# Performance work log

Measured on AMD Instinct MI355X. Metric: run time of the kernel, lower is better.

The kernel has to match this reference:

```python
import jax, jax.numpy as jnp
import numpy as np

B, IC, N = 32, 1, 64
KN, KS, PAD = 128, 65, 16
R, LAT = 8, 32
LEAK = 0.01
THETA_PRIOR = float(np.pi)
HW = N + 2 * PAD - KS + 1  # 32
OFFSETS = np.array([0, np.pi/4, np.pi/2, 3*np.pi/4, np.pi, -3*np.pi/4, -np.pi/2, -np.pi/4], dtype=np.float32)


def rotate_filters(w, n_rot):
    """Bilinear rotation of [O,I,k,k] filters for n_rot angles, matching
    F.affine_grid/F.grid_sample with align_corners=False, zero padding.
    Returns [O*n_rot, I, k, k] (rotation-major within each O block)."""
    O, I, k, _ = w.shape
    thetas = (2.0 * jnp.pi / n_rot) * jnp.arange(n_rot, dtype=jnp.float32)
    coords = (2.0 * jnp.arange(k, dtype=jnp.float32) + 1.0) / k - 1.0  # normalized, align_corners=False
    yy, xx = jnp.meshgrid(coords, coords, indexing='ij')  # [k,k]
    cos = jnp.cos(thetas)[:, None, None]
    sin = jnp.sin(thetas)[:, None, None]
    xs = cos * xx + sin * yy   # [R,k,k] sample x (normalized)
    ys = -sin * xx + cos * yy  # [R,k,k] sample y
    px = ((xs + 1.0) * k - 1.0) * 0.5  # pixel coords
    py = ((ys + 1.0) * k - 1.0) * 0.5
    x0 = jnp.floor(px); y0 = jnp.floor(py)
    wx = px - x0; wy = py - y0

    def gather(yi, xi):
        valid = (yi >= 0) & (yi < k) & (xi >= 0) & (xi < k)
        yc = jnp.clip(yi, 0, k - 1).astype(jnp.int32)
        xc = jnp.clip(xi, 0, k - 1).astype(jnp.int32)
        v = w[:, :, yc, xc]  # [O,I,R,k,k]
        return v * valid.astype(w.dtype)

    out = (gather(y0, x0) * (1 - wy) * (1 - wx)
           + gather(y0, x0 + 1) * (1 - wy) * wx
           + gather(y0 + 1, x0) * wy * (1 - wx)
           + gather(y0 + 1, x0 + 1) * wy * wx)  # [O,I,R,k,k]
    return jnp.transpose(out, (0, 2, 1, 3, 4)).reshape(O * n_rot, I, k, k)


def conv1x1(h, w, b):
    # h: [B,C,R,H,W], w: [O,C], b: [O] -- Conv3d with 1x1x1 kernel
    return jnp.einsum('bcrhw,oc->borhw', h, w) + b[None, :, None, None, None]


def _forward(x, w1, b1, w2, b2, wa, ba, wr, br, wz, bz, gumbel):
    tw = rotate_filters(w1[:, :, 0], R)  # [KN*R, IC, KS, KS]
    y = jax.lax.conv_general_dilated(
        x, tw, window_strides=(1, 1), padding=[(PAD, PAD), (PAD, PAD)],
        dimension_numbers=('NCHW', 'OIHW', 'NCHW'))
    Bn = y.shape[0]
    y = y.reshape(Bn, KN, R, HW, HW) + b1[None, :, None, None, None]
    xa = jax.nn.leaky_relu(y, LEAK)
    h = jax.nn.leaky_relu(conv1x1(xa, w2, b2), LEAK)
    attn = conv1x1(h, wa, ba)[:, 0]  # [B,R,H,W]
    offsets = jnp.asarray(OFFSETS)
    # Normal(0, theta_prior).log_prob(offsets)
    p_r = (-0.5 * (offsets / THETA_PRIOR) ** 2
           - jnp.log(THETA_PRIOR) - 0.5 * jnp.log(2.0 * jnp.pi))[:, None, None]  # [R,1,1]
    attn = attn + p_r  # broadcast over batch
    flat = attn.reshape(Bn, -1)
    q_t_r = jax.nn.log_softmax(flat, axis=1).reshape(attn.shape)
    a_sampled = jax.nn.softmax(flat + gumbel.reshape(Bn, -1), axis=-1).reshape(Bn, R, HW, HW)
    z = conv1x1(h, wz, bz)      # [B,2*LAT,R,H,W]
    theta = conv1x1(h, wr, br)  # [B,2,R,H,W]
    theta_mu = theta[:, 0] + offsets[None, :, None, None]
    theta = jnp.stack((theta_mu, theta[:, 1]), axis=1)
    return attn, q_t_r, p_r, a_sampled, offsets, theta, z


def setup_inputs():
    key = jax.random.key(0)
    ks = jax.random.split(key, 12)
    stdv1 = 1.0 / np.sqrt(IC * KS * KS)
    stdv2 = 1.0 / np.sqrt(KN)
    def unif(k, shape, a):
        return jax.random.uniform(k, shape, jnp.float32, -a, a)
    u = jax.random.uniform(ks[11], (B, R, HW, HW), jnp.float32, 1e-6, 1.0 - 1e-6)
    gumbel = -jnp.log(-jnp.log(u))
    return {
        'x': jax.random.normal(ks[0], (B, IC, N, N), jnp.float32),
        'w1': unif(ks[1], (KN, IC, 1, KS, KS), stdv1),
        'b1': unif(ks[2], (KN,), stdv1),
        'w2': unif(ks[3], (KN, KN), stdv2),
        'b2': unif(ks[4], (KN,), stdv2),
        'wa': unif(ks[5], (1, KN), stdv2),
        'ba': unif(ks[6], (1,), stdv2),
        'wr': unif(ks[7], (2, KN), stdv2),
        'br': unif(ks[8], (2,), stdv2),
        'wz': unif(ks[9], (2 * LAT, KN), stdv2),
        'bz': unif(ks[10], (2 * LAT,), stdv2),
        'gumbel': gumbel,
    }


def reference(x, w1, b1, w2, b2, wa, ba, wr, br, wz, bz, gumbel):
    return _forward(x, w1, b1, w2, b2, wa, ba, wr, br, wz, bz, gumbel)
```

## Files before the change

### kernel.cpp

```cpp
#include <hip/hip_runtime.h>
#include <hip/hip_bf16.h>

typedef unsigned int u32;
typedef unsigned short u16;

#define KYP 72
#define KPAD 4736
#define NK   74

#define OUT_ATTN 0
#define OUT_QTR  262144
#define OUT_PR   524288
#define OUT_AS   524296
#define OUT_OFF  786440
#define OUT_TH   786448
#define OUT_Z    1310736

typedef __attribute__((ext_vector_type(8))) short bf16x8;
typedef __attribute__((ext_vector_type(4))) float f32x4;

__device__ const float OFFS[8] = {
  0.0f,
  0.78539816339744830961f,
  1.57079632679489661923f,
  2.35619449019234492885f,
  3.14159265358979323846f,
 -2.35619449019234492885f,
 -1.57079632679489661923f,
 -0.78539816339744830961f
};

__device__ __forceinline__ float leaky_(float v){ return v >= 0.0f ? v : 0.01f*v; }

__device__ __forceinline__ u16 f2bf(float f){
  u32 x = __float_as_uint(f);
  u32 r = (x + 0x7FFFu + ((x >> 16) & 1u)) >> 16;
  return (u16)r;
}

__device__ __forceinline__ void gload_lds16(const void* g, void* l){
  __builtin_amdgcn_global_load_lds((const __attribute__((address_space(1))) u32*)g,
                                   (__attribute__((address_space(3))) u32*)l, 16, 0, 0);
}

#define BARRIER() { asm volatile("" ::: "memory"); __builtin_amdgcn_s_barrier(); asm volatile("" ::: "memory"); }
#define WAITV(N)  asm volatile("s_waitcnt vmcnt(" #N ")" ::: "memory")

__global__ __launch_bounds__(256) void xshift_kernel(const float* __restrict__ x, u16* __restrict__ xsh){
  int t = blockIdx.x*256 + threadIdx.x;
  if (t >= 393216) return;
  int c8  = t & 15;
  int u   = t >> 4;
  int row = u % 96;
  int v   = u / 96;
  int b   = v & 31;
  int s   = v >> 5;
  int iy = row - 16;
  u16 h[8];
#pragma unroll
  for (int j = 0; j < 8; ++j){
    int ix = c8*8 + j + s - 16;
    float val = 0.0f;
    if (iy >= 0 && iy < 64 && ix >= 0 && ix < 64) val = x[(b*64 + iy)*64 + ix];
    h[j] = f2bf(val);
  }
  uint4 pk;
  pk.x = (u32)h[0] | ((u32)h[1] << 16);
  pk.y = (u32)h[2] | ((u32)h[3] << 16);
  pk.z = (u32)h[4] | ((u32)h[5] << 16);
  pk.w = (u32)h[6] | ((u32)h[7] << 16);
  ((uint4*)xsh)[t] = pk;
}

__global__ __launch_bounds__(256) void rotate_kernel(const float* __restrict__ w1, u16* __restrict__ twb){
  __shared__ float wsh[4225];
  int n = blockIdx.x;
  int kn = n & 127, rot = n >> 7;
  for (int i = threadIdx.x; i < 4225; i += 256) wsh[i] = w1[kn*4225 + i];
  __syncthreads();
  float th  = 0.78539816339744830961f * (float)rot;
  float cth = cosf(th), sth = sinf(th);
  for (int t = threadIdx.x; t < KPAD; t += 256){
    int ky = t / KYP, kx = t - ky*KYP;
    u16 out = 0;
    if (ky < 65 && kx < 65){
      float yy = (2.0f*(float)ky + 1.0f)/65.0f - 1.0f;
      float xx = (2.0f*(float)kx + 1.0f)/65.0f - 1.0f;
      float xs  =  cth*xx + sth*yy;
      float ysv = -sth*xx + cth*yy;
      float px = ((xs  + 1.0f)*65.0f - 1.0f)*0.5f;
      float py = ((ysv + 1.0f)*65.0f - 1.0f)*0.5f;
      float x0 = floorf(px), y0 = floorf(py);
      float wx = px - x0, wy = py - y0;
      auto samp = [&](float yf, float xf)->float{
        bool valid = (yf >= 0.0f) && (yf < 65.0f) && (xf >= 0.0f) && (xf < 65.0f);
        int yc = (int)fminf(fmaxf(yf, 0.0f), 64.0f);
        int xc = (int)fminf(fmaxf(xf, 0.0f), 64.0f);
        return valid ? wsh[yc*65 + xc] : 0.0f;
      };
      float val = samp(y0,      x0     )*(1.0f-wy)*(1.0f-wx)
                + samp(y0,      x0+1.0f)*(1.0f-wy)*wx
                + samp(y0+1.0f, x0     )*wy*(1.0f-wx)
                + samp(y0+1.0f, x0+1.0f)*wy*wx;
      out = f2bf(val);
    }
    twb[(size_t)n*KPAD + t] = out;
  }
}

__global__ __launch_bounds__(512, 2) void gemm_kernel(const u16* __restrict__ xsh,
                                                      const u16* __restrict__ twb,
                                                      u16* __restrict__ ys){
  __shared__ u16 AsB[2*16384];
  __shared__ u16 BsB[2*16384];

  const int bid  = blockIdx.x;
  const int nblk = bid & 3, mblk = bid >> 2;
  const int t    = threadIdx.x;
  const int lane = t & 63, w = t >> 6;
  const int wr   = w >> 2, wn = w & 3;
  const int hi8  = (lane >> 4) << 3;

  const int sr  = t >> 3;
  const int j0e = (t & 7) * 8;
  const int jsw = j0e ^ ((sr & 7) << 3);
  const int bg  = mblk >> 4;
  const int ox2 = (mblk & 15) * 2;
  int aOff[4];
#pragma unroll
  for (int c = 0; c < 4; ++c){
    int i  = c*64 + sr;
    int ox = ox2 + (i >> 7);
    int s_ = ox & 7, colb = ox & ~7;
    int b_ = (bg << 2) + ((i & 127) >> 5);
    int oy = i & 31;
    aOff[c] = ((s_*32 + b_)*96 + oy)*128 + colb;
  }
  const u16* bPtr[4];
#pragma unroll
  for (int c = 0; c < 4; ++c){
    int nloc = c*64 + sr;
    bPtr[c] = twb + (size_t)(nblk*256 + nloc)*KPAD + jsw;
  }

  auto stageA4 = [&](int kt, u16* dstbase){
    int k = kt*64 + jsw;
    u32 ky = (u32)k / (u32)KYP;
    int kx0 = k - (int)ky*KYP;
    bool pad = (ky >= 65);
    int kofs = (int)ky*128 + kx0;
#pragma unroll
    for (int c = 0; c < 4; ++c){
      int gofs = pad ? 0 : (aOff[c] + kofs);
      gload_lds16(xsh + gofs, dstbase + c*4096 + w*512);
    }
  };
  auto stageB4 = [&](int kt, u16* dstbase){
#pragma unroll
    for (int c = 0; c < 4; ++c)
      gload_lds16(bPtr[c] + kt*64, dstbase + c*4096 + w*512);
  };

  f32x4 acc[8][4];
#pragma unroll
  for (int i = 0; i < 8; ++i)
#pragma unroll
    for (int j = 0; j < 4; ++j) acc[i][j] = (f32x4){0.f,0.f,0.f,0.f};
  bf16x8 amat[4][2], bmat[4][2];

  auto readA = [&](int mh, const char* Ab){
#pragma unroll
    for (int mj = 0; mj < 4; ++mj){
      int row = wr*128 + mh*64 + mj*16 + (lane & 15);
#pragma unroll
      for (int kk = 0; kk < 2; ++kk){
        int off = (row*128 + (kk*32 + hi8)*2) ^ ((row & 7) << 4);
        amat[mj][kk] = *(const bf16x8*)(Ab + off);
      }
    }
  };
  auto readB = [&](int nh, const char* Bb){
#pragma unroll
    for (int jn = 0; jn < 2; ++jn){
      int row = wn*64 + (nh*2 + jn)*16 + (lane & 15);
#pragma unroll
      for (int kk = 0; kk < 2; ++kk){
        int off = (row*128 + (kk*32 + hi8)*2) ^ ((row & 7) << 4);
        bmat[nh*2 + jn][kk] = *(const bf16x8*)(Bb + off);
      }
    }
  };
  auto mfma16 = [&](int MH, int NH){
    __builtin_amdgcn_s_setprio(1);
#pragma unroll
    for (int mj = 0; mj < 4; ++mj)
#pragma unroll
      for (int jn = 0; jn < 2; ++jn)
#pragma unroll
        for (int kk = 0; kk < 2; ++kk)
          acc[MH*4+mj][NH*2+jn] = __builtin_amdgcn_mfma_f32_16x16x32_bf16(
              amat[mj][kk], bmat[NH*2+jn][kk], acc[MH*4+mj][NH*2+jn], 0, 0, 0);
    __builtin_amdgcn_s_setprio(0);
  };

  u16* const A0 = AsB;
  u16* const B0 = BsB;
  u16* const A1 = AsB + 16384;
  u16* const B1 = BsB + 16384;

  stageA4(0, A0); stageB4(0, B0);

  for (int kc2 = 0; kc2 < NK; kc2 += 2){
    stageA4(kc2+1, A1);
    WAITV(4);
    BARRIER();
    readA(0, (const char*)A0); readB(0, (const char*)B0);
    mfma16(0, 0);
    BARRIER();
    stageB4(kc2+1, B1);
    readB(1, (const char*)B0);
    mfma16(0, 1);
    BARRIER();
    readA(1, (const char*)A0);
    mfma16(1, 1);
    BARRIER();
    mfma16(1, 0);
    BARRIER();
    const bool more = (kc2 + 2) < NK;
    if (more){ stageA4(kc2+2, A0); WAITV(4); }
    else     { WAITV(0); }
    BARRIER();
    readA(0, (const char*)A1); readB(0, (const char*)B1);
    mfma16(0, 0);
    BARRIER();
    if (more) stageB4(kc2+2, B0);
    readB(1, (const char*)B1);
    mfma16(0, 1);
    BARRIER();
    readA(1, (const char*)A1);
    mfma16(1, 1);
    BARRIER();
    mfma16(1, 0);
    BARRIER();
  }

  const int m_base = mblk*256 + wr*128;
  const int n_base = nblk*256 + wn*64;
  const int rsub = (lane >> 4) << 2;
  const int csub = lane & 15;
#pragma unroll
  for (int mf = 0; mf < 8; ++mf)
#pragma unroll
    for (int nf = 0; nf < 4; ++nf)
#pragma unroll
      for (int j = 0; j < 4; ++j){
        int m = m_base + mf*16 + rsub + j;
        int n = n_base + nf*16 + csub;
        ys[(size_t)m*1024 + n] = f2bf(acc[mf][nf][j]);
      }
}

__global__ __launch_bounds__(512) void mix_kernel(const u16* __restrict__ ys,
    const float* __restrict__ b1, const float* __restrict__ w2, const float* __restrict__ b2,
    const float* __restrict__ wa, const float* __restrict__ ba,
    const float* __restrict__ wr, const float* __restrict__ br,
    const float* __restrict__ wz, const float* __restrict__ bz,
    float* __restrict__ out){
  __shared__ __align__(16) u16 Ah[256*128];
  __shared__ __align__(16) u16 W2s[128*128];
  __shared__ __align__(16) u16 Wcs[80*128];
  __shared__ float b2s[128];
  __shared__ float bcs[80];

  const int blk = blockIdx.x;
  const int b   = blk >> 5, oy = blk & 31;
  const int t    = threadIdx.x;
  const int lane = t & 63;
  const int w    = t >> 6;

  {
    const int kn0 = (t & 15)*8;
    const int r_  = (t >> 4) & 7;
    float b1v[8];
#pragma unroll
    for (int j = 0; j < 8; ++j) b1v[j] = b1[kn0 + j];
#pragma unroll
    for (int i = 0; i < 8; ++i){
      int m_loc = 4*i + (t >> 7);
      int row_m = (((b >> 2)*32 + m_loc)*128) + (b & 3)*32 + oy;
      uint4 v = *(const uint4*)(ys + (size_t)row_m*1024 + r_*128 + kn0);
      u32 vv[4] = {v.x, v.y, v.z, v.w};
      u16 hh[8];
#pragma unroll
      for (int j = 0; j < 4; ++j){
        float lo = __uint_as_float(vv[j] << 16);
        float hi = __uint_as_float(vv[j] & 0xFFFF0000u);
        hh[2*j]   = f2bf(leaky_(lo + b1v[2*j]));
        hh[2*j+1] = f2bf(leaky_(hi + b1v[2*j+1]));
      }
      int Arow = r_*32 + m_loc;
      int off = (Arow*256 + kn0*2) ^ ((Arow & 7) << 4);
      uint4 pk;
      pk.x = (u32)hh[0] | ((u32)hh[1] << 16);
      pk.y = (u32)hh[2] | ((u32)hh[3] << 16);
      pk.z = (u32)hh[4] | ((u32)hh[5] << 16);
      pk.w = (u32)hh[6] | ((u32)hh[7] << 16);
      *(uint4*)((char*)Ah + off) = pk;
    }
  }
#pragma unroll
  for (int i = 0; i < 4; ++i){
    int ch = i*512 + t;
    int row = ch >> 4, kn0 = (ch & 15)*8;
    const float* src = w2 + row*128 + kn0;
    u16 hh[8];
#pragma unroll
    for (int j = 0; j < 8; ++j) hh[j] = f2bf(src[j]);
    int off = (row*256 + kn0*2) ^ ((row & 7) << 4);
    uint4 pk;
    pk.x = (u32)hh[0] | ((u32)hh[1] << 16);
    pk.y = (u32)hh[2] | ((u32)hh[3] << 16);
    pk.z = (u32)hh[4] | ((u32)hh[5] << 16);
    pk.w = (u32)hh[6] | ((u32)hh[7] << 16);
    *(uint4*)((char*)W2s + off) = pk;
  }
#pragma unroll
  for (int i = 0; i < 3; ++i){
    int ch = i*512 + t;
    if (ch < 1280){
      int row = ch >> 4, kn0 = (ch & 15)*8;
      const float* src = nullptr;
      if (row < 64)      src = wz + row*128 + kn0;
      else if (row == 64) src = wa + kn0;
      else if (row == 65) src = wr + kn0;
      else if (row == 66) src = wr + 128 + kn0;
      u16 hh[8];
#pragma unroll
      for (int j = 0; j < 8; ++j) hh[j] = src ? f2bf(src[j]) : (u16)0;
      int off = (row*256 + kn0*2) ^ ((row & 7) << 4);
      uint4 pk;
      pk.x = (u32)hh[0] | ((u32)hh[1] << 16);
      pk.y = (u32)hh[2] | ((u32)hh[3] << 16);
      pk.z = (u32)hh[4] | ((u32)hh[5] << 16);
      pk.w = (u32)hh[6] | ((u32)hh[7] << 16);
      *(uint4*)((char*)Wcs + off) = pk;
    }
  }
  if (t < 128) b2s[t] = b2[t];
  if (t < 80){
    float v = 0.0f;
    if (t < 64) v = bz[t];
    else if (t == 64) v = ba[0];
    else if (t == 65) v = br[0];
    else if (t == 66) v = br[1];
    bcs[t] = v;
  }
  __syncthreads();

  f32x4 acc1[2][8];
#pragma unroll
  for (int mf = 0; mf < 2; ++mf)
#pragma unroll
    for (int nf = 0; nf < 8; ++nf) acc1[mf][nf] = (f32x4){0.f,0.f,0.f,0.f};
#pragma unroll
  for (int kk = 0; kk < 128; kk += 32){
    int kb = (kk + ((lane >> 4) << 3))*2;
    bf16x8 a[2], bv[8];
#pragma unroll
    for (int mf = 0; mf < 2; ++mf){
      int row = w*32 + mf*16 + (lane & 15);
      int off = (row*256 + kb) ^ ((row & 7) << 4);
      a[mf] = *(const bf16x8*)((const char*)Ah + off);
    }
#pragma unroll
    for (int nf = 0; nf < 8; ++nf){
      int row = nf*16 + (lane & 15);
      int off = (row*256 + kb) ^ ((row & 7) << 4);
      bv[nf] = *(const bf16x8*)((const char*)W2s + off);
    }
#pragma unroll
    for (int mf = 0; mf < 2; ++mf)
#pragma unroll
      for (int nf = 0; nf < 8; ++nf)
        acc1[mf][nf] = __builtin_amdgcn_mfma_f32_16x16x32_bf16(a[mf], bv[nf], acc1[mf][nf], 0, 0, 0);
  }
  __syncthreads();

#pragma unroll
  for (int mf = 0; mf < 2; ++mf)
#pragma unroll
    for (int nf = 0; nf < 8; ++nf){
      int col = nf*16 + (lane & 15);
      float bb = b2s[col];
#pragma unroll
      for (int j = 0; j < 4; ++j){
        int row = w*32 + mf*16 + ((lane >> 4) << 2) + j;
        u16 hv = f2bf(leaky_(acc1[mf][nf][j] + bb));
        int off = (row*256 + col*2) ^ ((row & 7) << 4);
        *(u16*)((char*)Ah + off) = hv;
      }
    }
  __syncthreads();

  f32x4 acc2[2][5];
#pragma unroll
  for (int mf = 0; mf < 2; ++mf)
#pragma unroll
    for (int nf = 0; nf < 5; ++nf) acc2[mf][nf] = (f32x4){0.f,0.f,0.f,0.f};
#pragma unroll
  for (int kk = 0; kk < 128; kk += 32){
    int kb = (kk + ((lane >> 4) << 3))*2;
    bf16x8 a[2], bv[5];
#pragma unroll
    for (int mf = 0; mf < 2; ++mf){
      int row = w*32 + mf*16 + (lane & 15);
      int off = (row*256 + kb) ^ ((row & 7) << 4);
      a[mf] = *(const bf16x8*)((const char*)Ah + off);
    }
#pragma unroll
    for (int nf = 0; nf < 5; ++nf){
      int row = nf*16 + (lane & 15);
      int off = (row*256 + kb) ^ ((row & 7) << 4);
      bv[nf] = *(const bf16x8*)((const char*)Wcs + off);
    }
#pragma unroll
    for (int mf = 0; mf < 2; ++mf)
#pragma unroll
      for (int nf = 0; nf < 5; ++nf)
        acc2[mf][nf] = __builtin_amdgcn_mfma_f32_16x16x32_bf16(a[mf], bv[nf], acc2[mf][nf], 0, 0, 0);
  }

  const int r = w;
  float off_r = OFFS[r];
  float qn = off_r / 3.14159265358979323846f;
  float pr = -0.5f*qn*qn - 1.14472988584940017414f - 0.91893853320467274178f;
  const int pixb = oy*32;
#pragma unroll
  for (int mf = 0; mf < 2; ++mf)
#pragma unroll
    for (int nf = 0; nf < 5; ++nf){
      int c = nf*16 + (lane & 15);
#pragma unroll
      for (int j = 0; j < 4; ++j){
        int ox = mf*16 + ((lane >> 4) << 2) + j;
        float val = acc2[mf][nf][j];
        if (c < 64){
          out[OUT_Z + (size_t)b*524288 + (size_t)c*8192 + r*1024 + pixb + ox] = val + bcs[c];
        } else if (c == 64){
          out[OUT_ATTN + (size_t)(b*8 + r)*1024 + pixb + ox] = val + bcs[64] + pr;
        } else if (c == 65){
          out[OUT_TH + ((size_t)b*2)*8192 + r*1024 + pixb + ox] = val + bcs[65] + off_r;
        } else if (c == 66){
          out[OUT_TH + ((size_t)b*2 + 1)*8192 + r*1024 + pixb + ox] = val + bcs[66];
        }
      }
    }
}

__global__ __launch_bounds__(256) void softmax_kernel(const float* __restrict__ gumbel, float* __restrict__ out){
  __shared__ float a[8192];
  __shared__ float red[256];
  const int b = blockIdx.x, t = threadIdx.x;
  const float* attn = out + OUT_ATTN + (size_t)b*8192;
  float m = -3.0e38f;
  for (int i = t; i < 8192; i += 256){ float v = attn[i]; a[i] = v; m = fmaxf(m, v); }
  red[t] = m; __syncthreads();
#pragma unroll
  for (int s = 128; s > 0; s >>= 1){ if (t < s) red[t] = fmaxf(red[t], red[t+s]); __syncthreads(); }
  m = red[0]; __syncthreads();
  float s1 = 0.0f;
  for (int i = t; i < 8192; i += 256) s1 += expf(a[i] - m);
  red[t] = s1; __syncthreads();
#pragma unroll
  for (int s = 128; s > 0; s >>= 1){ if (t < s) red[t] += red[t+s]; __syncthreads(); }
  float lse = m + logf(red[0]);
  __syncthreads();
  float* q = out + OUT_QTR + (size_t)b*8192;
  for (int i = t; i < 8192; i += 256) q[i] = a[i] - lse;
  const float* g = gumbel + (size_t)b*8192;
  float m2 = -3.0e38f;
  for (int i = t; i < 8192; i += 256){ float v = a[i] + g[i]; a[i] = v; m2 = fmaxf(m2, v); }
  __syncthreads();
  red[t] = m2; __syncthreads();
#pragma unroll
  for (int s = 128; s > 0; s >>= 1){ if (t < s) red[t] = fmaxf(red[t], red[t+s]); __syncthreads(); }
  m2 = red[0]; __syncthreads();
  float s2 = 0.0f;
  for (int i = t; i < 8192; i += 256) s2 += expf(a[i] - m2);
  red[t] = s2; __syncthreads();
#pragma unroll
  for (int s = 128; s > 0; s >>= 1){ if (t < s) red[t] += red[t+s]; __syncthreads(); }
  float inv = 1.0f/red[0];
  float* as_ = out + OUT_AS + (size_t)b*8192;
  for (int i = t; i < 8192; i += 256) as_[i] = expf(a[i] - m2)*inv;
}

__global__ void tiny_kernel(float* __restrict__ out){
  int t = threadIdx.x;
  if (t < 8){
    float off = OFFS[t];
    out[OUT_OFF + t] = off;
    float qn = off / 3.14159265358979323846f;
    out[OUT_PR + t] = -0.5f*qn*qn - 1.14472988584940017414f - 0.91893853320467274178f;
  }
}

extern "C" void kernel_launch(void* const* d_in, const int* in_sizes, int n_in,
                              void* d_out, int out_size, void* d_ws, size_t ws_size,
                              hipStream_t stream){
  const float* x      = (const float*)d_in[0];
  const float* w1     = (const float*)d_in[1];
  const float* b1     = (const float*)d_in[2];
  const float* w2     = (const float*)d_in[3];
  const float* b2     = (const float*)d_in[4];
  const float* wa     = (const float*)d_in[5];
  const float* ba     = (const float*)d_in[6];
  const float* wr     = (const float*)d_in[7];
  const float* br     = (const float*)d_in[8];
  const float* wz     = (const float*)d_in[9];
  const float* bz     = (const float*)d_in[10];
  const float* gumbel = (const float*)d_in[11];
  float* out = (float*)d_out;

  u16* twb = (u16*)d_ws;
  u16* xsh = twb + (size_t)1024*KPAD;
  u16* ys  = xsh + (size_t)8*32*96*128;

  xshift_kernel <<<1536, 256, 0, stream>>>(x, xsh);
  rotate_kernel <<<1024, 256, 0, stream>>>(w1, twb);
  gemm_kernel   <<<512,  512, 0, stream>>>(xsh, twb, ys);
  mix_kernel    <<<1024, 512, 0, stream>>>(ys, b1, w2, b2, wa, ba, wr, br, wz, bz, out);
  softmax_kernel<<<32,   256, 0, stream>>>(gumbel, out);
  tiny_kernel   <<<1,    64,  0, stream>>>(out);
}
```

Before: 401.3 us.

## Restructure GEMM main loop into single-stage pipeline with explicit LDS waits

Rewrites the unrolled-by-two double-buffered K loop of the conv GEMM as a single-iteration loop that swaps buffers. The next tile's B and A loads are issued earlier, interleaved with the LDS reads of the current tile, and vmcnt waits are tightened. Each MFMA group is fenced with explicit lgkmcnt(0) waits and scheduling barriers. The intent is to overlap global-to-LDS prefetch with compute more evenly and stop the compiler from reordering MFMAs around LDS reads. The trade-off is extra barriers and one redundant load on the last iteration, with a B index clamp to keep it in bounds.

```diff
diff --git a/kernel.cpp b/kernel.cpp
--- a/kernel.cpp
+++ b/kernel.cpp
@@ -45,6 +45,8 @@
 
 #define BARRIER() { asm volatile("" ::: "memory"); __builtin_amdgcn_s_barrier(); asm volatile("" ::: "memory"); }
 #define WAITV(N)  asm volatile("s_waitcnt vmcnt(" #N ")" ::: "memory")
+#define LGK0()    { asm volatile("s_waitcnt lgkmcnt(0)" ::: "memory"); __builtin_amdgcn_sched_barrier(0); }
+#define SCHEDB()  __builtin_amdgcn_sched_barrier(0)
 
 __global__ __launch_bounds__(256) void xshift_kernel(const float* __restrict__ x, u16* __restrict__ xsh){
   int t = blockIdx.x*256 + threadIdx.x;
@@ -149,16 +151,19 @@
     int kx0 = k - (int)ky*KYP;
     bool pad = (ky >= 65);
     int kofs = (int)ky*128 + kx0;
-#pragma unroll
-    for (int c = 0; c < 4; ++c){
+    const int ord[4] = {0, 2, 1, 3};
+#pragma unroll
+    for (int ii = 0; ii < 4; ++ii){
+      int c = ord[ii];
       int gofs = pad ? 0 : (aOff[c] + kofs);
       gload_lds16(xsh + gofs, dstbase + c*4096 + w*512);
     }
   };
   auto stageB4 = [&](int kt, u16* dstbase){
+    int ktc = (kt < NK) ? kt : (NK-1);
 #pragma unroll
     for (int c = 0; c < 4; ++c)
-      gload_lds16(bPtr[c] + kt*64, dstbase + c*4096 + w*512);
+      gload_lds16(bPtr[c] + ktc*64, dstbase + c*4096 + w*512);
   };
 
   f32x4 acc[8][4];
@@ -208,39 +213,40 @@
   u16* const A1 = AsB + 16384;
   u16* const B1 = BsB + 16384;
 
-  stageA4(0, A0); stageB4(0, B0);
-
-  for (int kc2 = 0; kc2 < NK; kc2 += 2){
-    stageA4(kc2+1, A1);
-    WAITV(4);
-    BARRIER();
-    readA(0, (const char*)A0); readB(0, (const char*)B0);
+  stageB4(0, B0);
+  stageA4(0, A0);
+  WAITV(2);
+  BARRIER();
+
+  for (int kt = 0; kt < NK; ++kt){
+    u16* Ab = (kt & 1) ? A1 : A0;
+    u16* Bb = (kt & 1) ? B1 : B0;
+    u16* An = (kt & 1) ? A0 : A1;
+    u16* Bn = (kt & 1) ? B0 : B1;
+    readA(0, (const char*)Ab); readB(0, (const char*)Bb);
+    stageB4(kt+1, Bn);
+    BARRIER();
+    LGK0();
     mfma16(0, 0);
-    BARRIER();
-    stageB4(kc2+1, B1);
-    readB(1, (const char*)B0);
+    SCHEDB();
+    BARRIER();
+    readB(1, (const char*)Bb);
+    stageA4(kt+1, An);
+    BARRIER();
+    LGK0();
     mfma16(0, 1);
-    BARRIER();
-    readA(1, (const char*)A0);
+    SCHEDB();
+    WAITV(8);
+    BARRIER();
+    readA(1, (const char*)Ab);
+    BARRIER();
+    LGK0();
     mfma16(1, 1);
+    SCHEDB();
     BARRIER();
     mfma16(1, 0);
-    BARRIER();
-    const bool more = (kc2 + 2) < NK;
-    if (more){ stageA4(kc2+2, A0); WAITV(4); }
-    else     { WAITV(0); }
-    BARRIER();
-    readA(0, (const char*)A1); readB(0, (const char*)B1);
-    mfma16(0, 0);
-    BARRIER();
-    if (more) stageB4(kc2+2, B0);
-    readB(1, (const char*)B1);
-    mfma16(0, 1);
-    BARRIER();
-    readA(1, (const char*)A1);
-    mfma16(1, 1);
-    BARRIER();
-    mfma16(1, 0);
+    SCHEDB();
+    WAITV(2);
     BARRIER();
   }
 
```

Result: faster. 367.8 us (-8.4%).
